# Kernel tuning notes

Measured on AMD Instinct MI355X. Metric: run time of the kernel, lower is better.

Reference implementation:

```python
import jax, jax.numpy as jnp
import numpy as np
import math

H = 8  # num_heads

def setup_inputs() -> dict:
    key = jax.random.key(0)
    ks = jax.random.split(key, 12)
    B, N, M, k = 2, 8192, 8192, 32
    dq, dk, dv = 256, 256, 256
    s = 1.0 / math.sqrt(dq)
    inp = {
        'Q': jax.random.normal(ks[0], (B, N, dq), dtype=jnp.float32),
        'K': jax.random.normal(ks[1], (B, M, dk), dtype=jnp.float32),
        'neighbours': jax.random.randint(ks[2], (B, N, k), 0, M),
        'Wq': jax.random.normal(ks[3], (dq, dv), dtype=jnp.float32) * s,
        'bq': jnp.zeros((dv,), dtype=jnp.float32),
        'Wk': jax.random.normal(ks[4], (dk, dv), dtype=jnp.float32) * s,
        'bk': jnp.zeros((dv,), dtype=jnp.float32),
        'Wv': jax.random.normal(ks[5], (dk, dv), dtype=jnp.float32) * s,
        'bv': jnp.zeros((dv,), dtype=jnp.float32),
        'Wo': jax.random.normal(ks[6], (dv, dv), dtype=jnp.float32) * (1.0 / math.sqrt(dv)),
        'bo': jnp.zeros((dv,), dtype=jnp.float32),
    }
    return inp

def reference(Q, K, neighbours, Wq, bq, Wk, bk, Wv, bv, Wo, bo):
    B, N, _ = Q.shape
    dv = Wq.shape[1]
    ds = dv // H
    # project and split heads (contiguous channel chunks == reshape)
    Qh = (Q @ Wq + bq).reshape(B, N, H, ds)            # [B,N,H,ds]
    Kh = (K @ Wk + bk).reshape(B, -1, H, ds)           # [B,M,H,ds]
    Vh = (K @ Wv + bv).reshape(B, -1, H, ds)           # [B,M,H,ds]
    # gather per-node kNN neighbour keys/values: [B,N,k,H,ds]
    gather = jax.vmap(lambda x, idx: x[idx])
    Kn = gather(Kh, neighbours)
    Vn = gather(Vh, neighbours)
    # scale uses full latent size (faithful to original), not head dim
    scale = 1.0 / math.sqrt(dv)
    E = jnp.einsum('bnhd,bnkhd->bnhk', Qh, Kn) * scale  # [B,N,H,k]
    A = jax.nn.softmax(E, axis=-1)
    AV = jnp.einsum('bnhk,bnkhd->bnhd', A, Vn).reshape(B, N, dv)
    return AV @ Wo + bo
```

## Files before the change

kernel.cpp:

```cpp
#include <hip/hip_runtime.h>
#include <hip/hip_bf16.h>
#include <stdint.h>

typedef unsigned short u16;
typedef __attribute__((ext_vector_type(8))) short short8;
typedef __attribute__((ext_vector_type(4))) float f32x4;

__device__ __forceinline__ u16 f2bf(float f) {
    union { float f; unsigned int i; } v; v.f = f;
    unsigned int b = v.i;
    return (u16)((b + 0x7FFFu + ((b >> 16) & 1u)) >> 16);
}

__device__ __forceinline__ short8 cvt8(float4 a, float4 b) {
    union { __hip_bfloat162 h[4]; short8 s; } u;
    u.h[0] = __float22bfloat162_rn(make_float2(a.x, a.y));
    u.h[1] = __float22bfloat162_rn(make_float2(a.z, a.w));
    u.h[2] = __float22bfloat162_rn(make_float2(b.x, b.y));
    u.h[3] = __float22bfloat162_rn(make_float2(b.z, b.w));
    return u.s;
}

typedef const __attribute__((address_space(1))) void* as1cv;
typedef __attribute__((address_space(3))) void* as3v;
__device__ __forceinline__ void gload16(const void* g, void* l) {
    __builtin_amdgcn_global_load_lds((as1cv)g, (as3v)l, 16, 0, 0);
}

__device__ __forceinline__ void up2(unsigned int v, float& lo, float& hi) {
    union { unsigned int i; float f; } a, b;
    a.i = v << 16; b.i = v & 0xffff0000u;
    lo = a.f; hi = b.f;
}

__global__ __launch_bounds__(256) void wprep(
    const float* __restrict__ W0, const float* __restrict__ W1,
    const float* __restrict__ W2, const float* __restrict__ W3,
    u16* __restrict__ T0, u16* __restrict__ T1,
    u16* __restrict__ T2, u16* __restrict__ T3)
{
    const float* W = blockIdx.z == 0 ? W0 : blockIdx.z == 1 ? W1 : blockIdx.z == 2 ? W2 : W3;
    u16*        T  = blockIdx.z == 0 ? T0 : blockIdx.z == 1 ? T1 : blockIdx.z == 2 ? T2 : T3;
    __shared__ u16 ts[64][65];
    int k0 = blockIdx.x * 64, n0 = blockIdx.y * 64;
    int t = threadIdx.x;
    int r = t >> 2, cq = (t & 3) * 16;
    const float4* src = reinterpret_cast<const float4*>(W + (k0 + r) * 256 + n0 + cq);
    for (int u = 0; u < 4; ++u) {
        float4 v = src[u];
        int c = cq + u * 4;
        ts[r][c + 0] = f2bf(v.x); ts[r][c + 1] = f2bf(v.y);
        ts[r][c + 2] = f2bf(v.z); ts[r][c + 3] = f2bf(v.w);
    }
    __syncthreads();
    u16* dst = T + (n0 + r) * 256 + k0 + cq;
    for (int u = 0; u < 16; ++u) dst[u] = ts[cq + u][r];
}

__global__ __launch_bounds__(256) void gemm_proj(
    const float* __restrict__ Q, const float* __restrict__ K,
    const u16* __restrict__ Wtq, const u16* __restrict__ Wtk, const u16* __restrict__ Wtv,
    const float* __restrict__ bq, const float* __restrict__ bk, const float* __restrict__ bv,
    u16* __restrict__ Qh, u16* __restrict__ Kh, u16* __restrict__ Vh)
{
    int z = blockIdx.z;
    const float* Af   = (z == 0) ? Q   : K;
    const u16*   Wt   = (z == 0) ? Wtq : (z == 1) ? Wtk : Wtv;
    const float* bias = (z == 0) ? bq  : (z == 1) ? bk  : bv;
    u16*         C    = (z == 0) ? Qh  : (z == 1) ? Kh  : Vh;

    __shared__ float Asf[128 * 64];
    __shared__ u16   Bs[128 * 64];

    int t = threadIdx.x;
    int lane = t & 63, w = t >> 6;
    int row0 = blockIdx.x * 128, col0 = blockIdx.y * 128;
    int wr = (w >> 1) * 64, wc = (w & 1) * 64;
    int qd = lane >> 4, md = lane & 15;

    f32x4 acc[4][4] = {};

    for (int kt = 0; kt < 256; kt += 64) {
#pragma unroll
        for (int u = 0; u < 8; ++u) {
            int chunk = w * 8 + u;
            int s = chunk * 64 + lane;
            int r = s >> 4, c = s & 15;
            gload16(Af + (size_t)(row0 + r) * 256 + kt + ((c ^ (r & 15)) * 4),
                    (char*)Asf + chunk * 1024);
        }
#pragma unroll
        for (int u = 0; u < 4; ++u) {
            int chunk = w * 4 + u;
            int s = chunk * 64 + lane;
            int r = s >> 3, c = s & 7;
            gload16(Wt + (size_t)(col0 + r) * 256 + kt + ((c ^ (r & 7)) * 8),
                    (char*)Bs + chunk * 1024);
        }
        __syncthreads();
#pragma unroll
        for (int ks = 0; ks < 64; ks += 32) {
            short8 af[4], bf[4];
#pragma unroll
            for (int i = 0; i < 4; ++i) {
                int ar = wr + i * 16 + md;
                int c0 = (ks >> 2) + qd * 2;
                int x = ar & 15;
                float4 fa0 = reinterpret_cast<const float4*>(Asf)[ar * 16 + (c0 ^ x)];
                float4 fa1 = reinterpret_cast<const float4*>(Asf)[ar * 16 + ((c0 + 1) ^ x)];
                af[i] = cvt8(fa0, fa1);
            }
#pragma unroll
            for (int j = 0; j < 4; ++j) {
                int br = wc + j * 16 + md;
                int slot = ((ks >> 3) + qd) ^ (br & 7);
                bf[j] = reinterpret_cast<const short8*>(Bs)[br * 8 + slot];
            }
#pragma unroll
            for (int i = 0; i < 4; ++i)
#pragma unroll
                for (int j = 0; j < 4; ++j)
                    acc[i][j] = __builtin_amdgcn_mfma_f32_16x16x32_bf16(
                        af[i], bf[j], acc[i][j], 0, 0, 0);
        }
        __syncthreads();
    }

#pragma unroll
    for (int i = 0; i < 4; ++i)
#pragma unroll
        for (int j = 0; j < 4; ++j) {
            int col = col0 + wc + j * 16 + md;
            float b = bias[col];
#pragma unroll
            for (int r = 0; r < 4; ++r) {
                int row = row0 + wr + i * 16 + qd * 4 + r;
                C[(size_t)row * 256 + col] = f2bf(acc[i][j][r] + b);
            }
        }
}

__global__ __launch_bounds__(256) void gemm_out(
    const u16* __restrict__ Ab, const u16* __restrict__ Wt,
    const float* __restrict__ bias, float* __restrict__ Cout)
{
    __shared__ u16 As[64 * 64];
    __shared__ u16 Bs[128 * 64];

    int t = threadIdx.x;
    int lane = t & 63, w = t >> 6;
    int row0 = blockIdx.x * 64, col0 = blockIdx.y * 128;
    int wr = (w >> 1) * 32, wc = (w & 1) * 64;
    int qd = lane >> 4, md = lane & 15;

    f32x4 acc[2][4] = {};

    for (int kt = 0; kt < 256; kt += 64) {
#pragma unroll
        for (int u = 0; u < 2; ++u) {
            int chunk = w * 2 + u;
            int s = chunk * 64 + lane;
            int r = s >> 3, c = s & 7;
            gload16(Ab + (size_t)(row0 + r) * 256 + kt + ((c ^ (r & 7)) * 8),
                    (char*)As + chunk * 1024);
        }
#pragma unroll
        for (int u = 0; u < 4; ++u) {
            int chunk = w * 4 + u;
            int s = chunk * 64 + lane;
            int r = s >> 3, c = s & 7;
            gload16(Wt + (size_t)(col0 + r) * 256 + kt + ((c ^ (r & 7)) * 8),
                    (char*)Bs + chunk * 1024);
        }
        __syncthreads();
#pragma unroll
        for (int ks = 0; ks < 64; ks += 32) {
            short8 af[2], bf[4];
#pragma unroll
            for (int i = 0; i < 2; ++i) {
                int ar = wr + i * 16 + md;
                int slot = ((ks >> 3) + qd) ^ (ar & 7);
                af[i] = reinterpret_cast<const short8*>(As)[ar * 8 + slot];
            }
#pragma unroll
            for (int j = 0; j < 4; ++j) {
                int br = wc + j * 16 + md;
                int slot = ((ks >> 3) + qd) ^ (br & 7);
                bf[j] = reinterpret_cast<const short8*>(Bs)[br * 8 + slot];
            }
#pragma unroll
            for (int i = 0; i < 2; ++i)
#pragma unroll
                for (int j = 0; j < 4; ++j)
                    acc[i][j] = __builtin_amdgcn_mfma_f32_16x16x32_bf16(
                        af[i], bf[j], acc[i][j], 0, 0, 0);
        }
        __syncthreads();
    }

#pragma unroll
    for (int i = 0; i < 2; ++i)
#pragma unroll
        for (int j = 0; j < 4; ++j) {
            int col = col0 + wc + j * 16 + md;
            float b = bias[col];
#pragma unroll
            for (int r = 0; r < 4; ++r) {
                int row = row0 + wr + i * 16 + qd * 4 + r;
                Cout[(size_t)row * 256 + col] = acc[i][j][r] + b;
            }
        }
}

__global__ __launch_bounds__(256) void attn(
    const u16* __restrict__ Qh, const u16* __restrict__ Kh, const u16* __restrict__ Vh,
    const int* __restrict__ nbr, u16* __restrict__ AVb)
{
    __shared__ int jbs[4][32];

    int t = threadIdx.x;
    int w = t >> 6, lane = t & 63;
    int row = blockIdx.x * 4 + w;
    int b = row >> 13;
    int bbase = b << 13;

    int c8 = lane & 31;
    int jh = lane >> 5;

    if (lane < 32) {
        int ji = nbr[(size_t)row * 32 + lane];
        jbs[w][lane] = (bbase + ji) * 256;
    }

    float qf[8];
    {
        uint4 qw = *reinterpret_cast<const uint4*>(Qh + (size_t)row * 256 + c8 * 8);
        up2(qw.x, qf[0], qf[1]); up2(qw.y, qf[2], qf[3]);
        up2(qw.z, qf[4], qf[5]); up2(qw.w, qf[6], qf[7]);
    }

    float e16[16];
#pragma unroll
    for (int bb = 0; bb < 2; ++bb) {
        uint4 kw[8];
#pragma unroll
        for (int u = 0; u < 8; ++u) {
            int koff = jbs[w][jh * 16 + bb * 8 + u];
            kw[u] = *reinterpret_cast<const uint4*>(Kh + (size_t)koff + c8 * 8);
        }
#pragma unroll
        for (int u = 0; u < 8; ++u) {
            float k0, k1;
            float p = 0.f;
            up2(kw[u].x, k0, k1); p = fmaf(qf[0], k0, p); p = fmaf(qf[1], k1, p);
            up2(kw[u].y, k0, k1); p = fmaf(qf[2], k0, p); p = fmaf(qf[3], k1, p);
            up2(kw[u].z, k0, k1); p = fmaf(qf[4], k0, p); p = fmaf(qf[5], k1, p);
            up2(kw[u].w, k0, k1); p = fmaf(qf[6], k0, p); p = fmaf(qf[7], k1, p);
            p += __shfl_xor(p, 1);
            p += __shfl_xor(p, 2);
            e16[bb * 8 + u] = p * 0.0625f;
        }
    }

    float m = e16[0];
#pragma unroll
    for (int jj = 1; jj < 16; ++jj) m = fmaxf(m, e16[jj]);
    m = fmaxf(m, __shfl_xor(m, 32));
    float s = 0.f;
#pragma unroll
    for (int jj = 0; jj < 16; ++jj) { e16[jj] = __expf(e16[jj] - m); s += e16[jj]; }
    s += __shfl_xor(s, 32);
    float rs = 1.0f / s;
#pragma unroll
    for (int jj = 0; jj < 16; ++jj) e16[jj] *= rs;

    float acc[8] = {};
#pragma unroll
    for (int bb = 0; bb < 2; ++bb) {
        uint4 vv[8];
#pragma unroll
        for (int u = 0; u < 8; ++u) {
            int voff = jbs[w][jh * 16 + bb * 8 + u];
            vv[u] = *reinterpret_cast<const uint4*>(Vh + (size_t)voff + c8 * 8);
        }
#pragma unroll
        for (int u = 0; u < 8; ++u) {
            float v0, v1;
            float wgt = e16[bb * 8 + u];
            up2(vv[u].x, v0, v1); acc[0] = fmaf(wgt, v0, acc[0]); acc[1] = fmaf(wgt, v1, acc[1]);
            up2(vv[u].y, v0, v1); acc[2] = fmaf(wgt, v0, acc[2]); acc[3] = fmaf(wgt, v1, acc[3]);
            up2(vv[u].z, v0, v1); acc[4] = fmaf(wgt, v0, acc[4]); acc[5] = fmaf(wgt, v1, acc[5]);
            up2(vv[u].w, v0, v1); acc[6] = fmaf(wgt, v0, acc[6]); acc[7] = fmaf(wgt, v1, acc[7]);
        }
    }
#pragma unroll
    for (int u = 0; u < 8; ++u) acc[u] += __shfl_xor(acc[u], 32);

    if (lane < 32) {
        union { __hip_bfloat162 h[4]; uint4 u4; } o;
        o.h[0] = __float22bfloat162_rn(make_float2(acc[0], acc[1]));
        o.h[1] = __float22bfloat162_rn(make_float2(acc[2], acc[3]));
        o.h[2] = __float22bfloat162_rn(make_float2(acc[4], acc[5]));
        o.h[3] = __float22bfloat162_rn(make_float2(acc[6], acc[7]));
        *reinterpret_cast<uint4*>(AVb + (size_t)row * 256 + c8 * 8) = o.u4;
    }
}

extern "C" void kernel_launch(void* const* d_in, const int* in_sizes, int n_in,
                              void* d_out, int out_size, void* d_ws, size_t ws_size,
                              hipStream_t stream) {
    const float* Q   = (const float*)d_in[0];
    const float* K   = (const float*)d_in[1];
    const int*   nbr = (const int*)d_in[2];
    const float* Wq  = (const float*)d_in[3];
    const float* bq  = (const float*)d_in[4];
    const float* Wk  = (const float*)d_in[5];
    const float* bk  = (const float*)d_in[6];
    const float* Wv  = (const float*)d_in[7];
    const float* bv  = (const float*)d_in[8];
    const float* Wo  = (const float*)d_in[9];
    const float* bo  = (const float*)d_in[10];
    float* out = (float*)d_out;

    char* ws = (char*)d_ws;
    size_t off = 0;
    auto alloc = [&](size_t bytes) -> void* {
        void* p = ws + off;
        off += (bytes + 255) & ~(size_t)255;
        return p;
    };
    const size_t MN = 16384;
    u16* Wtq = (u16*)alloc(256 * 256 * 2);
    u16* Wtk = (u16*)alloc(256 * 256 * 2);
    u16* Wtv = (u16*)alloc(256 * 256 * 2);
    u16* Wto = (u16*)alloc(256 * 256 * 2);
    u16* Qh  = (u16*)alloc(MN * 256 * 2);
    u16* Kh  = (u16*)alloc(MN * 256 * 2);
    u16* Vh  = (u16*)alloc(MN * 256 * 2);
    u16* AVb = (u16*)alloc(MN * 256 * 2);

    wprep<<<dim3(4, 4, 4), 256, 0, stream>>>(Wq, Wk, Wv, Wo, Wtq, Wtk, Wtv, Wto);
    gemm_proj<<<dim3(128, 2, 3), 256, 0, stream>>>(Q, K, Wtq, Wtk, Wtv,
                                                   bq, bk, bv, Qh, Kh, Vh);
    attn<<<dim3(4096), 256, 0, stream>>>(Qh, Kh, Vh, nbr, AVb);
    gemm_out<<<dim3(256, 2), 256, 0, stream>>>(AVb, Wto, bo, out);
}
```

Measured before the change: 161.1 us.

## Retile projection GEMM to 64x256 blocks so fp32 A rows load once

The projection GEMM now has each block compute 64 rows across the full 256 output columns, with each wave owning 16 rows and 16 MFMA column tiles. Previously each 128-row A tile in fp32 was loaded and converted to bf16 twice, once per 128-column half. Now each A tile is read and converted once, which cuts fp32 global traffic for Q and K. In exchange each block reloads all of W per k-step, and each A fragment feeds only 16 MFMAs against one B read per MFMA, so the LDS-read-to-MFMA ratio is worse.

```diff
diff --git a/kernel.cpp b/kernel.cpp
--- a/kernel.cpp
+++ b/kernel.cpp
@@ -63,81 +63,69 @@
     const float* __restrict__ bq, const float* __restrict__ bk, const float* __restrict__ bv,
     u16* __restrict__ Qh, u16* __restrict__ Kh, u16* __restrict__ Vh)
 {
-    int z = blockIdx.z;
+    int z = blockIdx.y;
     const float* Af   = (z == 0) ? Q   : K;
     const u16*   Wt   = (z == 0) ? Wtq : (z == 1) ? Wtk : Wtv;
     const float* bias = (z == 0) ? bq  : (z == 1) ? bk  : bv;
     u16*         C    = (z == 0) ? Qh  : (z == 1) ? Kh  : Vh;
 
-    __shared__ float Asf[128 * 64];
-    __shared__ u16   Bs[128 * 64];
+    __shared__ float Asf[64 * 64];
+    __shared__ u16   Bs[256 * 64];
 
     int t = threadIdx.x;
     int lane = t & 63, w = t >> 6;
-    int row0 = blockIdx.x * 128, col0 = blockIdx.y * 128;
-    int wr = (w >> 1) * 64, wc = (w & 1) * 64;
+    int row0 = blockIdx.x * 64;
     int qd = lane >> 4, md = lane & 15;
 
-    f32x4 acc[4][4] = {};
+    f32x4 acc[16] = {};
 
     for (int kt = 0; kt < 256; kt += 64) {
 #pragma unroll
-        for (int u = 0; u < 8; ++u) {
-            int chunk = w * 8 + u;
+        for (int u = 0; u < 4; ++u) {
+            int chunk = w * 4 + u;
             int s = chunk * 64 + lane;
             int r = s >> 4, c = s & 15;
             gload16(Af + (size_t)(row0 + r) * 256 + kt + ((c ^ (r & 15)) * 4),
                     (char*)Asf + chunk * 1024);
         }
 #pragma unroll
-        for (int u = 0; u < 4; ++u) {
-            int chunk = w * 4 + u;
+        for (int u = 0; u < 8; ++u) {
+            int chunk = w * 8 + u;
             int s = chunk * 64 + lane;
             int r = s >> 3, c = s & 7;
-            gload16(Wt + (size_t)(col0 + r) * 256 + kt + ((c ^ (r & 7)) * 8),
+            gload16(Wt + (size_t)r * 256 + kt + ((c ^ (r & 7)) * 8),
                     (char*)Bs + chunk * 1024);
         }
         __syncthreads();
 #pragma unroll
         for (int ks = 0; ks < 64; ks += 32) {
-            short8 af[4], bf[4];
-#pragma unroll
-            for (int i = 0; i < 4; ++i) {
-                int ar = wr + i * 16 + md;
-                int c0 = (ks >> 2) + qd * 2;
-                int x = ar & 15;
-                float4 fa0 = reinterpret_cast<const float4*>(Asf)[ar * 16 + (c0 ^ x)];
-                float4 fa1 = reinterpret_cast<const float4*>(Asf)[ar * 16 + ((c0 + 1) ^ x)];
-                af[i] = cvt8(fa0, fa1);
+            int ar = w * 16 + md;
+            int c0 = (ks >> 2) + qd * 2;
+            int x = ar & 15;
+            float4 fa0 = reinterpret_cast<const float4*>(Asf)[ar * 16 + (c0 ^ x)];
+            float4 fa1 = reinterpret_cast<const float4*>(Asf)[ar * 16 + ((c0 + 1) ^ x)];
+            short8 af = cvt8(fa0, fa1);
+#pragma unroll
+            for (int j = 0; j < 16; ++j) {
+                int br = j * 16 + md;
+                int slot = ((ks >> 3) + qd) ^ (br & 7);
+                short8 bf = reinterpret_cast<const short8*>(Bs)[br * 8 + slot];
+                acc[j] = __builtin_amdgcn_mfma_f32_16x16x32_bf16(af, bf, acc[j], 0, 0, 0);
             }
-#pragma unroll
-            for (int j = 0; j < 4; ++j) {
-                int br = wc + j * 16 + md;
-                int slot = ((ks >> 3) + qd) ^ (br & 7);
-                bf[j] = reinterpret_cast<const short8*>(Bs)[br * 8 + slot];
-            }
-#pragma unroll
-            for (int i = 0; i < 4; ++i)
-#pragma unroll
-                for (int j = 0; j < 4; ++j)
-                    acc[i][j] = __builtin_amdgcn_mfma_f32_16x16x32_bf16(
-                        af[i], bf[j], acc[i][j], 0, 0, 0);
         }
         __syncthreads();
     }
 
 #pragma unroll
-    for (int i = 0; i < 4; ++i)
-#pragma unroll
-        for (int j = 0; j < 4; ++j) {
-            int col = col0 + wc + j * 16 + md;
-            float b = bias[col];
-#pragma unroll
-            for (int r = 0; r < 4; ++r) {
-                int row = row0 + wr + i * 16 + qd * 4 + r;
-                C[(size_t)row * 256 + col] = f2bf(acc[i][j][r] + b);
-            }
-        }
+    for (int j = 0; j < 16; ++j) {
+        int col = j * 16 + md;
+        float b = bias[col];
+#pragma unroll
+        for (int r = 0; r < 4; ++r) {
+            int row = row0 + w * 16 + qd * 4 + r;
+            C[(size_t)row * 256 + col] = f2bf(acc[j][r] + b);
+        }
+    }
 }
 
 __global__ __launch_bounds__(256) void gemm_out(
@@ -340,8 +328,8 @@
     u16* AVb = (u16*)alloc(MN * 256 * 2);
 
     wprep<<<dim3(4, 4, 4), 256, 0, stream>>>(Wq, Wk, Wv, Wo, Wtq, Wtk, Wtv, Wto);
-    gemm_proj<<<dim3(128, 2, 3), 256, 0, stream>>>(Q, K, Wtq, Wtk, Wtv,
-                                                   bq, bk, bv, Qh, Kh, Vh);
+    gemm_proj<<<dim3(256, 3), 256, 0, stream>>>(Q, K, Wtq, Wtk, Wtv,
+                                                bq, bk, bv, Qh, Kh, Vh);
     attn<<<dim3(4096), 256, 0, stream>>>(Qh, Kh, Vh, nbr, AVb);
     gemm_out<<<dim3(256, 2), 256, 0, stream>>>(AVb, Wto, bo, out);
 }
```

After: 164.5 us. 2.1% more time.

## Split attention into separate score and weighted-value kernels with interleaved row mapping

Applied to the files above, without the earlier changes.

Splits the fused gather-attention kernel into a score/softmax kernel that writes fp32 attention weights to a workspace buffer and a second kernel that reads them back and gathers V. It also remaps blocks so consecutive blocks alternate between the two batches. The split lowers per-kernel register pressure and separates the K and V gather traffic. In exchange it adds a launch plus a 16 MB fp32 write and read of the weights, and reloads the neighbour indices.

```diff
diff --git a/kernel.cpp b/kernel.cpp
--- a/kernel.cpp
+++ b/kernel.cpp
@@ -212,17 +212,24 @@
         }
 }
 
-__global__ __launch_bounds__(256) void attn(
-    const u16* __restrict__ Qh, const u16* __restrict__ Kh, const u16* __restrict__ Vh,
-    const int* __restrict__ nbr, u16* __restrict__ AVb)
+__device__ __forceinline__ int attn_row(int blk, int w) {
+    int g = blk & 7;
+    int batch = g >> 2;
+    int group = (blk >> 3) * 4 + (g & 3);
+    return batch * 8192 + group * 4 + w;
+}
+
+__global__ __launch_bounds__(256) void attn_score(
+    const u16* __restrict__ Qh, const u16* __restrict__ Kh,
+    const int* __restrict__ nbr, float* __restrict__ Wgt)
 {
     __shared__ int jbs[4][32];
+    __shared__ float wsm[4][256];
 
     int t = threadIdx.x;
     int w = t >> 6, lane = t & 63;
-    int row = blockIdx.x * 4 + w;
-    int b = row >> 13;
-    int bbase = b << 13;
+    int row = attn_row(blockIdx.x, w);
+    int bbase = (row >> 13) << 13;
 
     int c8 = lane & 31;
     int jh = lane >> 5;
@@ -271,8 +278,52 @@
     for (int jj = 0; jj < 16; ++jj) { e16[jj] = __expf(e16[jj] - m); s += e16[jj]; }
     s += __shfl_xor(s, 32);
     float rs = 1.0f / s;
-#pragma unroll
-    for (int jj = 0; jj < 16; ++jj) e16[jj] *= rs;
+
+    if ((c8 & 3) == 0) {
+        int h = c8 >> 2;
+#pragma unroll
+        for (int jj = 0; jj < 16; ++jj)
+            wsm[w][h * 32 + jh * 16 + jj] = e16[jj] * rs;
+    }
+    __syncthreads();
+
+    {
+        float4 v = *reinterpret_cast<const float4*>(&wsm[w][lane * 4]);
+        *reinterpret_cast<float4*>(Wgt + (size_t)row * 256 + lane * 4) = v;
+    }
+}
+
+__global__ __launch_bounds__(256) void attn_av(
+    const u16* __restrict__ Vh, const int* __restrict__ nbr,
+    const float* __restrict__ Wgt, u16* __restrict__ AVb)
+{
+    __shared__ int jbs[4][32];
+
+    int t = threadIdx.x;
+    int w = t >> 6, lane = t & 63;
+    int row = attn_row(blockIdx.x, w);
+    int bbase = (row >> 13) << 13;
+
+    int c8 = lane & 31;
+    int jh = lane >> 5;
+    int h = c8 >> 2;
+
+    if (lane < 32) {
+        int ji = nbr[(size_t)row * 32 + lane];
+        jbs[w][lane] = (bbase + ji) * 256;
+    }
+
+    float e16[16];
+    {
+        const float4* wp = reinterpret_cast<const float4*>(
+            Wgt + (size_t)row * 256 + h * 32 + jh * 16);
+#pragma unroll
+        for (int q = 0; q < 4; ++q) {
+            float4 v = wp[q];
+            e16[q * 4 + 0] = v.x; e16[q * 4 + 1] = v.y;
+            e16[q * 4 + 2] = v.z; e16[q * 4 + 3] = v.w;
+        }
+    }
 
     float acc[8] = {};
 #pragma unroll
@@ -297,11 +348,11 @@
     for (int u = 0; u < 8; ++u) acc[u] += __shfl_xor(acc[u], 32);
 
     if (lane < 32) {
-        union { __hip_bfloat162 h[4]; uint4 u4; } o;
-        o.h[0] = __float22bfloat162_rn(make_float2(acc[0], acc[1]));
-        o.h[1] = __float22bfloat162_rn(make_float2(acc[2], acc[3]));
-        o.h[2] = __float22bfloat162_rn(make_float2(acc[4], acc[5]));
-        o.h[3] = __float22bfloat162_rn(make_float2(acc[6], acc[7]));
+        union { __hip_bfloat162 h2[4]; uint4 u4; } o;
+        o.h2[0] = __float22bfloat162_rn(make_float2(acc[0], acc[1]));
+        o.h2[1] = __float22bfloat162_rn(make_float2(acc[2], acc[3]));
+        o.h2[2] = __float22bfloat162_rn(make_float2(acc[4], acc[5]));
+        o.h2[3] = __float22bfloat162_rn(make_float2(acc[6], acc[7]));
         *reinterpret_cast<uint4*>(AVb + (size_t)row * 256 + c8 * 8) = o.u4;
     }
 }
@@ -338,10 +389,12 @@
     u16* Kh  = (u16*)alloc(MN * 256 * 2);
     u16* Vh  = (u16*)alloc(MN * 256 * 2);
     u16* AVb = (u16*)alloc(MN * 256 * 2);
+    float* Wgt = (float*)alloc(MN * 256 * 4);
 
     wprep<<<dim3(4, 4, 4), 256, 0, stream>>>(Wq, Wk, Wv, Wo, Wtq, Wtk, Wtv, Wto);
     gemm_proj<<<dim3(128, 2, 3), 256, 0, stream>>>(Q, K, Wtq, Wtk, Wtv,
                                                    bq, bk, bv, Qh, Kh, Vh);
-    attn<<<dim3(4096), 256, 0, stream>>>(Qh, Kh, Vh, nbr, AVb);
+    attn_score<<<dim3(4096), 256, 0, stream>>>(Qh, Kh, nbr, Wgt);
+    attn_av<<<dim3(4096), 256, 0, stream>>>(Vh, nbr, Wgt, AVb);
     gemm_out<<<dim3(256, 2), 256, 0, stream>>>(AVb, Wto, bo, out);
 }
```

Result: faster. 153.4 us (-4.8%).
